# Performance work log

Hardware: AMD Instinct MI355X
Metric: run time of the kernel (lower is better)

The kernel has to match this reference:

```python
import jax, jax.numpy as jnp
import numpy as np

HEADS = 24
HEAD_DIM = 96
SPARSE_N = 4
ROPE_FREQ = 10000.0


def _rope_axis(x, pos, scale):
    # x: (s, b, h, D) with D even; pos: (s,) integer positions along one axis
    D = x.shape[-1]
    inv_freq = 1.0 / (ROPE_FREQ ** (jnp.arange(0, D, 2, dtype=jnp.float32) / D))
    t = pos.astype(jnp.float32) / scale
    freqs = t[:, None] * inv_freq[None, :]            # (s, D/2)
    emb = jnp.concatenate([freqs, freqs], axis=-1)    # (s, D)
    cos = jnp.cos(emb)[:, None, None, :]              # broadcast over (b, h)
    sin = jnp.sin(emb)[:, None, None, :]
    x1, x2 = jnp.split(x, 2, axis=-1)
    rot = jnp.concatenate([-x2, x1], axis=-1)         # rotate_half
    return x * cos + rot * sin


def _rope3d(x, frame, height, width, scales=(1.0, 1.0, 1.0)):
    # x: (s, b, h, d); head dim is split into 3 equal chunks for t/h/w axes
    s, b, h, d = x.shape
    D = d // 3
    tt, hh, ww = jnp.meshgrid(jnp.arange(frame), jnp.arange(height), jnp.arange(width), indexing='ij')
    pos_t, pos_h, pos_w = tt.reshape(-1), hh.reshape(-1), ww.reshape(-1)
    return jnp.concatenate([
        _rope_axis(x[..., :D], pos_t, scales[0]),
        _rope_axis(x[..., D:2 * D], pos_h, scales[1]),
        _rope_axis(x[..., 2 * D:], pos_w, scales[2]),
    ], axis=-1)


def setup_inputs() -> dict:
    key = jax.random.key(0)
    ks = jax.random.split(key, 9)
    frame, height, width, b = 8, 16, 16, 4
    s = frame * height * width          # 2048
    dim = HEADS * HEAD_DIM              # 2304
    w_scale = 0.02
    return {
        'hidden_states': jax.random.normal(ks[0], (s, b, dim), jnp.float32),
        'wq': jax.random.normal(ks[1], (dim, dim), jnp.float32) * w_scale,
        'bq': jnp.zeros((dim,), jnp.float32),
        'wk': jax.random.normal(ks[2], (dim, dim), jnp.float32) * w_scale,
        'bk': jnp.zeros((dim,), jnp.float32),
        'wv': jax.random.normal(ks[3], (dim, dim), jnp.float32) * w_scale,
        'bv': jnp.zeros((dim,), jnp.float32),
        'wo': jax.random.normal(ks[4], (dim, dim), jnp.float32) * w_scale,
        'bo': jnp.zeros((dim,), jnp.float32),
        'frame': frame,
        'height': height,
        'width': width,
    }


def reference(hidden_states, wq, bq, wk, bk, wv, bv, wo, bo, frame, height, width):
    # hidden_states: (s, b, dim) in SBH layout, self-attention path (no seq-parallel)
    s, b, dim = hidden_states.shape
    n = SPARSE_N

    q = hidden_states @ wq + bq
    k = hidden_states @ wk + bk
    v = hidden_states @ wv + bv

    # 3D RoPE on q/k, per-head
    q = _rope3d(q.reshape(s, b, HEADS, HEAD_DIM), frame, height, width).reshape(s, b, dim)
    k = _rope3d(k.reshape(s, b, HEADS, HEAD_DIM), frame, height, width).reshape(s, b, dim)

    # _sparse_1d (sparse_group=False): pad s to multiple of n*n, then
    # '(g k) b d -> g (k b) d' == contiguous reshape
    pad_len = (-s) % (n * n)
    sp_s = (s + pad_len) // n
    sp_b = n * b

    def sparse(x):
        if pad_len:
            x = jnp.pad(x, ((0, pad_len), (0, 0), (0, 0)))
        return x.reshape(sp_s, sp_b, dim)

    q, k, v = sparse(q), sparse(k), sparse(v)

    # 's b (h d) -> b h s d'
    def to_bhsd(x):
        return x.reshape(sp_s, sp_b, HEADS, HEAD_DIM).transpose(1, 2, 0, 3)

    qh, kh, vh = to_bhsd(q), to_bhsd(k), to_bhsd(v)

    # scaled dot-product attention (no mask, no dropout, non-causal)
    scale = HEAD_DIM ** -0.5
    scores = jnp.einsum('bhqd,bhkd->bhqk', qh, kh) * scale
    attn = jax.nn.softmax(scores, axis=-1)
    out = jnp.einsum('bhqk,bhkd->bhqd', attn, vh)

    # 'b h s d -> s b (h d)', reverse sparse rearrange, drop padding
    out = out.transpose(2, 0, 1, 3).reshape(sp_s, sp_b, dim)
    out = out.reshape(sp_s * n, b, dim)[:s]

    # to_out[0] linear, to_out[1] dropout (identity in eval), rescale_output_factor=1
    return out @ wo + bo
```

## Files before the change

### kernel.cpp

```cpp
#include <hip/hip_runtime.h>
#include <hip/hip_bf16.h>

typedef __attribute__((ext_vector_type(8))) __bf16 bf16x8;
typedef __attribute__((ext_vector_type(4))) __bf16 bf16x4;
typedef __attribute__((ext_vector_type(4))) float  f32x4;

#define DIM   2304
#define NH    24
#define HD    96
#define SPS   512

__device__ __forceinline__ void gload16(const void* gp, void* lp) {
  __builtin_amdgcn_global_load_lds(
      (__attribute__((address_space(1))) void*)(unsigned long long)gp,
      (__attribute__((address_space(3))) void*)lp, 16, 0, 0);
}

__global__ __launch_bounds__(256) void pack_w_kernel(
    const float* __restrict__ wq, const float* __restrict__ wk,
    const float* __restrict__ wv, const float* __restrict__ wo,
    __bf16* __restrict__ dqkv, __bf16* __restrict__ dwo)
{
  __shared__ float t[64][65];
  const int z = blockIdx.z;
  const float* src = (z == 0) ? wq : (z == 1) ? wk : (z == 2) ? wv : wo;
  __bf16* dst = (z < 3) ? (dqkv + (size_t)z * DIM * DIM) : dwo;
  const int n0 = blockIdx.x * 64, k0 = blockIdx.y * 64;
  const int tx = threadIdx.x & 63, ty = threadIdx.x >> 6;
#pragma unroll
  for (int j = 0; j < 64; j += 4)
    t[ty + j][tx] = src[(size_t)(k0 + ty + j) * DIM + n0 + tx];
  __syncthreads();
#pragma unroll
  for (int j = 0; j < 64; j += 4)
    dst[(size_t)(n0 + ty + j) * DIM + k0 + tx] = (__bf16)t[tx][ty + j];
}

__global__ __launch_bounds__(256) void pack_hs_kernel(
    const float4* __restrict__ src, bf16x4* __restrict__ dst)
{
  const int i = blockIdx.x * 256 + threadIdx.x;
  const float4 f = src[i];
  bf16x4 o = { (__bf16)f.x, (__bf16)f.y, (__bf16)f.z, (__bf16)f.w };
  dst[i] = o;
}


template<int NJ>
__device__ __forceinline__ void stage_half(
    const __bf16* __restrict__ X, __bf16* lX, int r0, int k0,
    int srow, int schunk, int dslot)
{
#pragma unroll
  for (int j = 0; j < NJ; ++j)
    gload16(X + (size_t)(r0 + j * 64 + srow) * DIM + k0 + schunk,
            lX + (j * 64 + srow) * 64 + dslot);
}

template<int MF, int H, int Q, bool LA, bool LB>
__device__ __forceinline__ void phase8(
    const char* ab, const char* bb, int wm, int wn, int laneA0, int laneA1,
    bf16x8 (&a)[MF][2], bf16x8 (&bq)[2][2][2], f32x4 (&acc)[2 * MF][4])
{
  if (LA) {
#pragma unroll
    for (int fm = 0; fm < MF; ++fm) {
      a[fm][0] = *(const bf16x8*)(ab + (wm * (MF * 32) + H * (MF * 16) + fm * 16) * 128 + laneA0);
      a[fm][1] = *(const bf16x8*)(ab + (wm * (MF * 32) + H * (MF * 16) + fm * 16) * 128 + laneA1);
    }
  }
  if (LB) {
#pragma unroll
    for (int fn = 0; fn < 2; ++fn) {
      bq[Q][fn][0] = *(const bf16x8*)(bb + (wn * 64 + Q * 32 + fn * 16) * 128 + laneA0);
      bq[Q][fn][1] = *(const bf16x8*)(bb + (wn * 64 + Q * 32 + fn * 16) * 128 + laneA1);
    }
  }
  __builtin_amdgcn_s_barrier();
  asm volatile("s_waitcnt lgkmcnt(0)" ::: "memory");
  __builtin_amdgcn_s_setprio(1);
#pragma unroll
  for (int fm = 0; fm < MF; ++fm)
#pragma unroll
    for (int fn = 0; fn < 2; ++fn)
#pragma unroll
      for (int kk = 0; kk < 2; ++kk)
        acc[H * MF + fm][Q * 2 + fn] = __builtin_amdgcn_mfma_f32_16x16x32_bf16(
            a[fm][kk], bq[Q][fn][kk], acc[H * MF + fm][Q * 2 + fn], 0, 0, 0);
  __builtin_amdgcn_s_setprio(0);
  __builtin_amdgcn_s_barrier();
}

template<int EPI>
__global__ __launch_bounds__(512, 2) void gemm8p_kernel(
    const __bf16* __restrict__ A, const __bf16* __restrict__ B,
    const float* __restrict__ b0, const float* __restrict__ b1, const float* __restrict__ b2,
    __bf16* __restrict__ o0, __bf16* __restrict__ o1, __bf16* __restrict__ o2,
    float* __restrict__ fout)
{
  constexpr int MF = (EPI == 0) ? 4 : 2;
  constexpr int MROWS = MF * 64;
  __shared__ __align__(16) __bf16 As[2][MROWS * 64];
  __shared__ __align__(16) __bf16 Bs[2][256 * 64];
  __shared__ float tcos[640], tsin[640];
  const int tid = threadIdx.x;
  if (EPI == 0) {
    for (int i = tid; i < 640; i += 512) {
      int pos, jj = i & 15;
      if (i < 128)      pos = i >> 4;
      else if (i < 384) pos = (i - 128) >> 4;
      else              pos = (i - 384) >> 4;
      const float invf = exp2f(-(float)jj * 0.83048202372184059f);
      float s, c;
      sincosf((float)pos * invf, &s, &c);
      tcos[i] = c; tsin[i] = s;
    }
  }
  const int wid = tid >> 6, l = tid & 63;
  const int lq = l & 15, lg = l >> 4;
  const int wm = wid >> 2, wn = wid & 3;
  const int bid = blockIdx.x;
  const int xcd = bid & 7, local = bid >> 3;
  int m0, n0;
  if (EPI == 0) {
    m0 = (xcd * 4 + (local & 3)) * 256;
    n0 = (local >> 2) * 256;
  } else {
    m0 = (xcd * 8 + (local & 7)) * 128;
    n0 = (local >> 3) * 256;
  }
  const int srow = tid >> 3;
  const int schunk = ((tid & 7) ^ (srow & 7)) * 8;
  const int dslot = (tid & 7) * 8;
  const int laneA0 = lq * 128 + ((lg * 16) ^ ((lq & 7) << 4));
  const int laneA1 = lq * 128 + ((64 + lg * 16) ^ ((lq & 7) << 4));

  f32x4 acc[2 * MF][4] = {};
  bf16x8 a[MF][2], bq[2][2][2];

  stage_half<MF>(A, As[0], m0, 0, srow, schunk, dslot);
  stage_half<4>(B, Bs[0], n0, 0, srow, schunk, dslot);
  stage_half<MF>(A, As[1], m0, 64, srow, schunk, dslot);
  stage_half<4>(B, Bs[1], n0, 64, srow, schunk, dslot);
  if (EPI == 0) asm volatile("s_waitcnt vmcnt(8)" ::: "memory");
  else          asm volatile("s_waitcnt vmcnt(6)" ::: "memory");
  __builtin_amdgcn_s_barrier();

  const char* a0p = (const char*)&As[0][0];
  const char* b0p = (const char*)&Bs[0][0];
  const char* a1p = (const char*)&As[1][0];
  const char* b1p = (const char*)&Bs[1][0];

#define TILE_STAGED(AP, BP, SA, SB, KN)                                          \
  phase8<MF, 0, 0, true,  true >(AP, BP, wm, wn, laneA0, laneA1, a, bq, acc);    \
  phase8<MF, 0, 1, false, true >(AP, BP, wm, wn, laneA0, laneA1, a, bq, acc);    \
  stage_half<4>(B, SB, n0, KN, srow, schunk, dslot);                             \
  phase8<MF, 1, 1, true,  false>(AP, BP, wm, wn, laneA0, laneA1, a, bq, acc);    \
  stage_half<MF>(A, SA, m0, KN, srow, schunk, dslot);                            \
  phase8<MF, 1, 0, false, false>(AP, BP, wm, wn, laneA0, laneA1, a, bq, acc);    \
  if (EPI == 0) asm volatile("s_waitcnt vmcnt(8)" ::: "memory");                 \
  else          asm volatile("s_waitcnt vmcnt(6)" ::: "memory");                 \
  __builtin_amdgcn_s_barrier();

#define TILE_PLAIN(AP, BP)                                                       \
  phase8<MF, 0, 0, true,  true >(AP, BP, wm, wn, laneA0, laneA1, a, bq, acc);    \
  phase8<MF, 0, 1, false, true >(AP, BP, wm, wn, laneA0, laneA1, a, bq, acc);    \
  phase8<MF, 1, 1, true,  false>(AP, BP, wm, wn, laneA0, laneA1, a, bq, acc);    \
  phase8<MF, 1, 0, false, false>(AP, BP, wm, wn, laneA0, laneA1, a, bq, acc);

  for (int tt = 0; tt < 34; tt += 2) {
    TILE_STAGED(a0p, b0p, As[0], Bs[0], (tt + 2) * 64)
    TILE_STAGED(a1p, b1p, As[1], Bs[1], (tt + 3) * 64)
  }
  TILE_PLAIN(a0p, b0p)
  asm volatile("s_waitcnt vmcnt(0)" ::: "memory");
  __builtin_amdgcn_s_barrier();
  TILE_PLAIN(a1p, b1p)
#undef TILE_STAGED
#undef TILE_PLAIN

  if (EPI == 0) {
    const int mat = n0 / DIM;
    const int nb = n0 - mat * DIM;
    const float* bias = (mat == 0) ? b0 : (mat == 1) ? b1 : b2;
    __bf16* outp = (mat == 0) ? o0 : (mat == 1) ? o1 : o2;
#pragma unroll
    for (int mr = 0; mr < 8; ++mr) {
      const int gq = (m0 + wm * 128 + mr * 16) >> 4;
      const int si = gq * 4 + lg;
      const int pos3[3] = { si >> 8, (si >> 4) & 15, si & 15 };
#pragma unroll
      for (int p = 0; p < 2; ++p) {
        const int nlo = nb + wn * 64 + (2 * p) * 16 + lq;
        const int nhi = nlo + 16;
        const int hlo = nlo / HD, dlo = nlo - hlo * HD;
        const int hhi = nhi / HD, dhi = nhi - hhi * HD;
        const float blo = bias[nlo], bhi = bias[nhi];
        float c = 1.f, s = 0.f;
        if (mat < 2) {
          const int cix = dlo >> 5;
          const int toff = ((cix == 0) ? 0 : (cix == 1) ? 128 : 384) + pos3[cix] * 16 + lq;
          c = tcos[toff]; s = tsin[toff];
        }
#pragma unroll
        for (int r = 0; r < 4; ++r) {
          const int bp = lg * 4 + r;
          const float x1 = acc[mr][2 * p][r] + blo;
          const float x2 = acc[mr][2 * p + 1][r] + bhi;
          float y1 = x1, y2 = x2;
          if (mat < 2) { y1 = x1 * c - x2 * s; y2 = x2 * c + x1 * s; }
          outp[((size_t)(bp * NH + hlo) * SPS + gq) * HD + dlo] = (__bf16)y1;
          outp[((size_t)(bp * NH + hhi) * SPS + gq) * HD + dhi] = (__bf16)y2;
        }
      }
    }
  } else {
#pragma unroll
    for (int mr = 0; mr < 4; ++mr) {
      const int rbase = m0 + wm * 64 + mr * 16;
#pragma unroll
      for (int nr = 0; nr < 4; ++nr) {
        const int n = n0 + wn * 64 + nr * 16 + lq;
        const float bia = b0[n];
#pragma unroll
        for (int r = 0; r < 4; ++r)
          fout[(size_t)(rbase + lg * 4 + r) * DIM + n] = acc[mr][nr][r] + bia;
      }
    }
  }
}

__global__ __launch_bounds__(256) void attn_kernel(
    const __bf16* __restrict__ q, const __bf16* __restrict__ k,
    const __bf16* __restrict__ v, __bf16* __restrict__ ao)
{
  __shared__ __bf16 Vt[96 * 72];
  __shared__ __bf16 Pl[4][16 * 72];
  const int tid = threadIdx.x;
  const int w = tid >> 6, l = tid & 63;
  const int lq = l & 15, lg = l >> 4;
  const int bid = blockIdx.x;
  const int swz = (bid & 7) * 384 + (bid >> 3);
  const int qt = swz & 7;
  const int h  = (swz >> 3) % NH;
  const int bp = swz / (NH * 8);
  const size_t bh = ((size_t)bp * NH + h) * SPS;
  const __bf16* qb = q + bh * HD;
  const __bf16* kb = k + bh * HD;
  const __bf16* vb = v + bh * HD;
  bf16x8 qf[3];
  {
    const __bf16* qr = qb + (size_t)(qt * 64 + w * 16 + lq) * HD + lg * 8;
    qf[0] = *(const bf16x8*)(qr);
    qf[1] = *(const bf16x8*)(qr + 32);
    qf[2] = *(const bf16x8*)(qr + 64);
  }
  const float sc = 0.10206207261596575f * 1.4426950408889634f;
  float m_run = -1e30f, l_run = 0.f;
  f32x4 o[6] = {};
  for (int kb0 = 0; kb0 < SPS; kb0 += 64) {
    __syncthreads();
#pragma unroll
    for (int p = 0; p < 3; ++p) {
      const int lin = p * 256 + tid;
      const int row = lin / 12, c8 = (lin % 12) * 8;
      bf16x8 vv = *(const bf16x8*)(vb + (size_t)(kb0 + row) * HD + c8);
#pragma unroll
      for (int j = 0; j < 8; ++j) Vt[(c8 + j) * 72 + row] = vv[j];
    }
    __syncthreads();
    f32x4 st[4];
#pragma unroll
    for (int t2 = 0; t2 < 4; ++t2) {
      const __bf16* kr = kb + (size_t)(kb0 + t2 * 16 + lq) * HD + lg * 8;
      bf16x8 k0f = *(const bf16x8*)(kr);
      bf16x8 k1f = *(const bf16x8*)(kr + 32);
      bf16x8 k2f = *(const bf16x8*)(kr + 64);
      f32x4 s = {};
      s = __builtin_amdgcn_mfma_f32_16x16x32_bf16(k0f, qf[0], s, 0, 0, 0);
      s = __builtin_amdgcn_mfma_f32_16x16x32_bf16(k1f, qf[1], s, 0, 0, 0);
      s = __builtin_amdgcn_mfma_f32_16x16x32_bf16(k2f, qf[2], s, 0, 0, 0);
      st[t2] = s;
    }
    float tmax = -1e30f;
#pragma unroll
    for (int t2 = 0; t2 < 4; ++t2)
#pragma unroll
      for (int r = 0; r < 4; ++r) tmax = fmaxf(tmax, st[t2][r]);
    tmax = fmaxf(tmax, __shfl_xor(tmax, 16));
    tmax = fmaxf(tmax, __shfl_xor(tmax, 32));
    tmax *= sc;
    const float m_new = fmaxf(m_run, tmax);
    const float alpha = exp2f(m_run - m_new);
    float tsum = 0.f;
#pragma unroll
    for (int t2 = 0; t2 < 4; ++t2) {
      bf16x4 pb;
#pragma unroll
      for (int r = 0; r < 4; ++r) {
        const float p = exp2f(st[t2][r] * sc - m_new);
        tsum += p;
        pb[r] = (__bf16)p;
      }
      *(bf16x4*)&Pl[w][lq * 72 + t2 * 16 + lg * 4] = pb;
    }
    tsum += __shfl_xor(tsum, 16);
    tsum += __shfl_xor(tsum, 32);
    l_run = l_run * alpha + tsum;
    m_run = m_new;
    float al[4];
#pragma unroll
    for (int r = 0; r < 4; ++r) al[r] = __shfl(alpha, lg * 4 + r);
#pragma unroll
    for (int ni = 0; ni < 6; ++ni)
#pragma unroll
      for (int r = 0; r < 4; ++r) o[ni][r] *= al[r];
#pragma unroll
    for (int ks = 0; ks < 2; ++ks) {
      bf16x8 pa = *(const bf16x8*)&Pl[w][lq * 72 + ks * 32 + lg * 8];
#pragma unroll
      for (int ni = 0; ni < 6; ++ni) {
        bf16x8 vf = *(const bf16x8*)&Vt[(ni * 16 + lq) * 72 + ks * 32 + lg * 8];
        o[ni] = __builtin_amdgcn_mfma_f32_16x16x32_bf16(pa, vf, o[ni], 0, 0, 0);
      }
    }
  }
  float linv[4];
#pragma unroll
  for (int r = 0; r < 4; ++r) linv[r] = 1.f / __shfl(l_run, lg * 4 + r);
#pragma unroll
  for (int ni = 0; ni < 6; ++ni)
#pragma unroll
    for (int r = 0; r < 4; ++r) {
      const int gq = qt * 64 + w * 16 + lg * 4 + r;
      const int d = ni * 16 + lq;
      ao[(size_t)(gq * 16 + bp) * DIM + h * HD + d] = (__bf16)(o[ni][r] * linv[r]);
    }
}

extern "C" void kernel_launch(void* const* d_in, const int* in_sizes, int n_in,
                              void* d_out, int out_size, void* d_ws, size_t ws_size,
                              hipStream_t stream) {
  const float* hs = (const float*)d_in[0];
  const float* wq = (const float*)d_in[1];
  const float* bq = (const float*)d_in[2];
  const float* wk = (const float*)d_in[3];
  const float* bk = (const float*)d_in[4];
  const float* wv = (const float*)d_in[5];
  const float* bv = (const float*)d_in[6];
  const float* wo = (const float*)d_in[7];
  const float* bo = (const float*)d_in[8];
  float* out = (float*)d_out;

  char* ws = (char*)d_ws;
  __bf16* wqkvT = (__bf16*)(ws);
  __bf16* woT   = (__bf16*)(ws + 31850496);
  __bf16* hsb   = (__bf16*)(ws + 42467328);
  __bf16* qb    = (__bf16*)(ws + 80216064);
  __bf16* kbuf  = (__bf16*)(ws + 117964800);
  __bf16* vbuf  = (__bf16*)(ws + 155713536);
  __bf16* ao    = hsb;

  pack_w_kernel<<<dim3(36, 36, 4), 256, 0, stream>>>(wq, wk, wv, wo, wqkvT, woT);
  pack_hs_kernel<<<18432, 256, 0, stream>>>((const float4*)hs, (bf16x4*)hsb);
  gemm8p_kernel<0><<<864, 512, 0, stream>>>(hsb, wqkvT, bq, bk, bv, qb, kbuf, vbuf, nullptr);
  attn_kernel<<<3072, 256, 0, stream>>>(qb, kbuf, vbuf, ao);
  gemm8p_kernel<1><<<576, 512, 0, stream>>>(ao, woT, bo, nullptr, nullptr, nullptr, nullptr, nullptr, out);
}
```

Before: 570.6 us.

## Software-pipeline LDS fragment loads across MFMA phases in GEMM main loop

The per-phase load→barrier→wait-all→MFMA structure is replaced by a software-pipelined schedule. The next A/B fragments are read from LDS while the current MFMAs run, using double-buffered register sets, partial lgkmcnt waits and sched_barrier fences to pin the instruction order. Launch bounds drop from 2 to 1 block per CU so the extra live fragment registers fit. This aims to hide LDS latency behind matrix math, at the cost of lower occupancy and a more fragile hand-counted wait schedule.

```diff
diff --git a/kernel.cpp b/kernel.cpp
--- a/kernel.cpp
+++ b/kernel.cpp
@@ -9,6 +9,11 @@
 #define NH    24
 #define HD    96
 #define SPS   512
+
+#define SBAR() __builtin_amdgcn_sched_barrier(0)
+#define BARR() __builtin_amdgcn_s_barrier()
+#define LGKM(n) asm volatile("s_waitcnt lgkmcnt(%0)" :: "n"(n) : "memory")
+#define VMC(n)  asm volatile("s_waitcnt vmcnt(%0)"  :: "n"(n) : "memory")
 
 __device__ __forceinline__ void gload16(const void* gp, void* lp) {
   __builtin_amdgcn_global_load_lds(
@@ -57,49 +62,21 @@
             lX + (j * 64 + srow) * 64 + dslot);
 }
 
-template<int MF, int H, int Q, bool LA, bool LB>
-__device__ __forceinline__ void phase8(
-    const char* ab, const char* bb, int wm, int wn, int laneA0, int laneA1,
-    bf16x8 (&a)[MF][2], bf16x8 (&bq)[2][2][2], f32x4 (&acc)[2 * MF][4])
-{
-  if (LA) {
-#pragma unroll
-    for (int fm = 0; fm < MF; ++fm) {
-      a[fm][0] = *(const bf16x8*)(ab + (wm * (MF * 32) + H * (MF * 16) + fm * 16) * 128 + laneA0);
-      a[fm][1] = *(const bf16x8*)(ab + (wm * (MF * 32) + H * (MF * 16) + fm * 16) * 128 + laneA1);
-    }
-  }
-  if (LB) {
-#pragma unroll
-    for (int fn = 0; fn < 2; ++fn) {
-      bq[Q][fn][0] = *(const bf16x8*)(bb + (wn * 64 + Q * 32 + fn * 16) * 128 + laneA0);
-      bq[Q][fn][1] = *(const bf16x8*)(bb + (wn * 64 + Q * 32 + fn * 16) * 128 + laneA1);
-    }
-  }
-  __builtin_amdgcn_s_barrier();
-  asm volatile("s_waitcnt lgkmcnt(0)" ::: "memory");
-  __builtin_amdgcn_s_setprio(1);
-#pragma unroll
-  for (int fm = 0; fm < MF; ++fm)
-#pragma unroll
-    for (int fn = 0; fn < 2; ++fn)
-#pragma unroll
-      for (int kk = 0; kk < 2; ++kk)
-        acc[H * MF + fm][Q * 2 + fn] = __builtin_amdgcn_mfma_f32_16x16x32_bf16(
-            a[fm][kk], bq[Q][fn][kk], acc[H * MF + fm][Q * 2 + fn], 0, 0, 0);
-  __builtin_amdgcn_s_setprio(0);
-  __builtin_amdgcn_s_barrier();
-}
-
 template<int EPI>
-__global__ __launch_bounds__(512, 2) void gemm8p_kernel(
+__global__ __launch_bounds__(512, 1) void gemm8p_kernel(
     const __bf16* __restrict__ A, const __bf16* __restrict__ B,
-    const float* __restrict__ b0, const float* __restrict__ b1, const float* __restrict__ b2,
+    const float* __restrict__ b0, const float* __restrict__ b1v, const float* __restrict__ b2,
     __bf16* __restrict__ o0, __bf16* __restrict__ o1, __bf16* __restrict__ o2,
     float* __restrict__ fout)
 {
   constexpr int MF = (EPI == 0) ? 4 : 2;
   constexpr int MROWS = MF * 64;
+  constexpr int AL = 2 * MF;
+  constexpr int L_P0 = AL + 4;
+  constexpr int L_P1 = AL;
+  constexpr int L_P2 = AL + 4;
+  constexpr int V_PRO = MF + 4;
+
   __shared__ __align__(16) __bf16 As[2][MROWS * 64];
   __shared__ __align__(16) __bf16 Bs[2][256 * 64];
   __shared__ float tcos[640], tsin[640];
@@ -115,6 +92,7 @@
       sincosf((float)pos * invf, &s, &c);
       tcos[i] = c; tsin[i] = s;
     }
+    LGKM(0);
   }
   const int wid = tid >> 6, l = tid & 63;
   const int lq = l & 15, lg = l >> 4;
@@ -136,56 +114,80 @@
   const int laneA1 = lq * 128 + ((64 + lg * 16) ^ ((lq & 7) << 4));
 
   f32x4 acc[2 * MF][4] = {};
-  bf16x8 a[MF][2], bq[2][2][2];
+  bf16x8 aX[MF][2], aY[MF][2], b0A[2][2], b0B[2][2], b1[2][2];
+
+#define LOAD_A(dst, bufp, Hh) do { _Pragma("unroll")                            \
+  for (int fm = 0; fm < MF; ++fm) {                                             \
+    dst[fm][0] = *(const bf16x8*)((bufp) + (wm * (MF * 32) + (Hh) * (MF * 16) + fm * 16) * 128 + laneA0); \
+    dst[fm][1] = *(const bf16x8*)((bufp) + (wm * (MF * 32) + (Hh) * (MF * 16) + fm * 16) * 128 + laneA1); } } while (0)
+
+#define LOAD_B(dst, bufp, Qq) do { _Pragma("unroll")                            \
+  for (int fn = 0; fn < 2; ++fn) {                                              \
+    dst[fn][0] = *(const bf16x8*)((bufp) + (wn * 64 + (Qq) * 32 + fn * 16) * 128 + laneA0); \
+    dst[fn][1] = *(const bf16x8*)((bufp) + (wn * 64 + (Qq) * 32 + fn * 16) * 128 + laneA1); } } while (0)
+
+#define MFMA8(aset, bset, Hh, Qq) do {                                          \
+  __builtin_amdgcn_s_setprio(1); _Pragma("unroll")                              \
+  for (int fm = 0; fm < MF; ++fm) _Pragma("unroll")                             \
+    for (int fn = 0; fn < 2; ++fn) _Pragma("unroll")                            \
+      for (int kk = 0; kk < 2; ++kk)                                            \
+        acc[(Hh) * MF + fm][(Qq) * 2 + fn] = __builtin_amdgcn_mfma_f32_16x16x32_bf16( \
+            aset[fm][kk], bset[fn][kk], acc[(Hh) * MF + fm][(Qq) * 2 + fn], 0, 0, 0); \
+  __builtin_amdgcn_s_setprio(0); } while (0)
 
   stage_half<MF>(A, As[0], m0, 0, srow, schunk, dslot);
   stage_half<4>(B, Bs[0], n0, 0, srow, schunk, dslot);
   stage_half<MF>(A, As[1], m0, 64, srow, schunk, dslot);
   stage_half<4>(B, Bs[1], n0, 64, srow, schunk, dslot);
-  if (EPI == 0) asm volatile("s_waitcnt vmcnt(8)" ::: "memory");
-  else          asm volatile("s_waitcnt vmcnt(6)" ::: "memory");
-  __builtin_amdgcn_s_barrier();
-
+  VMC(V_PRO);
+  BARR();
   const char* a0p = (const char*)&As[0][0];
   const char* b0p = (const char*)&Bs[0][0];
   const char* a1p = (const char*)&As[1][0];
   const char* b1p = (const char*)&Bs[1][0];
-
-#define TILE_STAGED(AP, BP, SA, SB, KN)                                          \
-  phase8<MF, 0, 0, true,  true >(AP, BP, wm, wn, laneA0, laneA1, a, bq, acc);    \
-  phase8<MF, 0, 1, false, true >(AP, BP, wm, wn, laneA0, laneA1, a, bq, acc);    \
-  stage_half<4>(B, SB, n0, KN, srow, schunk, dslot);                             \
-  phase8<MF, 1, 1, true,  false>(AP, BP, wm, wn, laneA0, laneA1, a, bq, acc);    \
-  stage_half<MF>(A, SA, m0, KN, srow, schunk, dslot);                            \
-  phase8<MF, 1, 0, false, false>(AP, BP, wm, wn, laneA0, laneA1, a, bq, acc);    \
-  if (EPI == 0) asm volatile("s_waitcnt vmcnt(8)" ::: "memory");                 \
-  else          asm volatile("s_waitcnt vmcnt(6)" ::: "memory");                 \
-  __builtin_amdgcn_s_barrier();
-
-#define TILE_PLAIN(AP, BP)                                                       \
-  phase8<MF, 0, 0, true,  true >(AP, BP, wm, wn, laneA0, laneA1, a, bq, acc);    \
-  phase8<MF, 0, 1, false, true >(AP, BP, wm, wn, laneA0, laneA1, a, bq, acc);    \
-  phase8<MF, 1, 1, true,  false>(AP, BP, wm, wn, laneA0, laneA1, a, bq, acc);    \
-  phase8<MF, 1, 0, false, false>(AP, BP, wm, wn, laneA0, laneA1, a, bq, acc);
+  LOAD_A(aX, a0p, 0);
+  LOAD_B(b0A, b0p, 0);
+  LOAD_B(b1, b0p, 1);
+  SBAR();
+
+#define STEADY_TILE(ACURP, BCURP, ANXTP, BNXTP, SADST, SBDST, B0CUR, B0NXT, KNOFF, DOSTG, GATEN) \
+  BARR(); LOAD_A(aY, ACURP, 1); SBAR(); LGKM(L_P0); SBAR(); MFMA8(aX, B0CUR, 0, 0);  \
+  BARR(); SBAR(); LGKM(L_P1); SBAR(); MFMA8(aX, b1, 0, 1);                            \
+  BARR();                                                                              \
+  if (DOSTG) stage_half<4>(B, SBDST, n0, KNOFF, srow, schunk, dslot);                  \
+  VMC(GATEN); BARR();                                                                  \
+  LOAD_A(aX, ANXTP, 0); LOAD_B(B0NXT, BNXTP, 0); SBAR(); LGKM(L_P2); SBAR();           \
+  MFMA8(aY, b1, 1, 1);                                                                 \
+  BARR();                                                                              \
+  if (DOSTG) stage_half<MF>(A, SADST, m0, KNOFF, srow, schunk, dslot);                 \
+  LOAD_B(b1, BNXTP, 1); SBAR(); MFMA8(aY, B0CUR, 1, 0);
+
+#define FINAL_TILE(ACURP, B0CUR)                                                      \
+  BARR(); LOAD_A(aY, ACURP, 1); SBAR(); LGKM(L_P0); SBAR(); MFMA8(aX, B0CUR, 0, 0);  \
+  BARR(); SBAR(); LGKM(L_P1); SBAR(); MFMA8(aX, b1, 0, 1);                            \
+  BARR(); SBAR(); LGKM(0); SBAR(); MFMA8(aY, b1, 1, 1);                               \
+  BARR(); SBAR(); MFMA8(aY, B0CUR, 1, 0);
 
   for (int tt = 0; tt < 34; tt += 2) {
-    TILE_STAGED(a0p, b0p, As[0], Bs[0], (tt + 2) * 64)
-    TILE_STAGED(a1p, b1p, As[1], Bs[1], (tt + 3) * 64)
-  }
-  TILE_PLAIN(a0p, b0p)
-  asm volatile("s_waitcnt vmcnt(0)" ::: "memory");
-  __builtin_amdgcn_s_barrier();
-  TILE_PLAIN(a1p, b1p)
-#undef TILE_STAGED
-#undef TILE_PLAIN
+    STEADY_TILE(a0p, b0p, a1p, b1p, As[0], Bs[0], b0A, b0B, (tt + 2) * 64, 1, 4)
+    STEADY_TILE(a1p, b1p, a0p, b0p, As[1], Bs[1], b0B, b0A, (tt + 3) * 64, 1, 4)
+  }
+  STEADY_TILE(a0p, b0p, a1p, b1p, As[0], Bs[0], b0A, b0B, 0, 0, 0)
+  FINAL_TILE(a1p, b0B)
+
+#undef STEADY_TILE
+#undef FINAL_TILE
+#undef LOAD_A
+#undef LOAD_B
+#undef MFMA8
 
   if (EPI == 0) {
     const int mat = n0 / DIM;
     const int nb = n0 - mat * DIM;
-    const float* bias = (mat == 0) ? b0 : (mat == 1) ? b1 : b2;
+    const float* bias = (mat == 0) ? b0 : (mat == 1) ? b1v : b2;
     __bf16* outp = (mat == 0) ? o0 : (mat == 1) ? o1 : o2;
 #pragma unroll
-    for (int mr = 0; mr < 8; ++mr) {
+    for (int mr = 0; mr < 2 * MF; ++mr) {
       const int gq = (m0 + wm * 128 + mr * 16) >> 4;
       const int si = gq * 4 + lg;
       const int pos3[3] = { si >> 8, (si >> 4) & 15, si & 15 };
@@ -216,7 +218,7 @@
     }
   } else {
 #pragma unroll
-    for (int mr = 0; mr < 4; ++mr) {
+    for (int mr = 0; mr < 2 * MF; ++mr) {
       const int rbase = m0 + wm * 64 + mr * 16;
 #pragma unroll
       for (int nr = 0; nr < 4; ++nr) {
```

Result: slower. 1.558 ms (+173.0%).

## Store V transposed from QKV GEMM and read it directly in attention

Applied to the files above, without the earlier changes.

The QKV projection epilogue now writes V in a head-dim-major (transposed) layout, so the attention kernel can load V fragments straight from global memory instead of staging and transposing them through shared memory. This removes the per-tile V transpose and its two block barriers. MFMA sections are also wrapped in s_setprio to favour matrix issue. The costs are strided 2-byte scattered stores in the GEMM epilogue for V, and repeated global (L2) reads of V by every wave without LDS reuse.

```diff
diff --git a/kernel.cpp b/kernel.cpp
--- a/kernel.cpp
+++ b/kernel.cpp
@@ -209,8 +209,13 @@
           const float x2 = acc[mr][2 * p + 1][r] + bhi;
           float y1 = x1, y2 = x2;
           if (mat < 2) { y1 = x1 * c - x2 * s; y2 = x2 * c + x1 * s; }
-          outp[((size_t)(bp * NH + hlo) * SPS + gq) * HD + dlo] = (__bf16)y1;
-          outp[((size_t)(bp * NH + hhi) * SPS + gq) * HD + dhi] = (__bf16)y2;
+          if (mat == 2) {
+            outp[((size_t)(bp * NH + hlo) * HD + dlo) * SPS + gq] = (__bf16)y1;
+            outp[((size_t)(bp * NH + hhi) * HD + dhi) * SPS + gq] = (__bf16)y2;
+          } else {
+            outp[((size_t)(bp * NH + hlo) * SPS + gq) * HD + dlo] = (__bf16)y1;
+            outp[((size_t)(bp * NH + hhi) * SPS + gq) * HD + dhi] = (__bf16)y2;
+          }
         }
       }
     }
@@ -232,9 +237,8 @@
 
 __global__ __launch_bounds__(256) void attn_kernel(
     const __bf16* __restrict__ q, const __bf16* __restrict__ k,
-    const __bf16* __restrict__ v, __bf16* __restrict__ ao)
-{
-  __shared__ __bf16 Vt[96 * 72];
+    const __bf16* __restrict__ vT, __bf16* __restrict__ ao)
+{
   __shared__ __bf16 Pl[4][16 * 72];
   const int tid = threadIdx.x;
   const int w = tid >> 6, l = tid & 63;
@@ -244,10 +248,10 @@
   const int qt = swz & 7;
   const int h  = (swz >> 3) % NH;
   const int bp = swz / (NH * 8);
-  const size_t bh = ((size_t)bp * NH + h) * SPS;
-  const __bf16* qb = q + bh * HD;
-  const __bf16* kb = k + bh * HD;
-  const __bf16* vb = v + bh * HD;
+  const size_t bh = (size_t)bp * NH + h;
+  const __bf16* qb = q + bh * SPS * HD;
+  const __bf16* kb = k + bh * SPS * HD;
+  const __bf16* vb = vT + bh * HD * SPS;
   bf16x8 qf[3];
   {
     const __bf16* qr = qb + (size_t)(qt * 64 + w * 16 + lq) * HD + lg * 8;
@@ -259,17 +263,8 @@
   float m_run = -1e30f, l_run = 0.f;
   f32x4 o[6] = {};
   for (int kb0 = 0; kb0 < SPS; kb0 += 64) {
-    __syncthreads();
-#pragma unroll
-    for (int p = 0; p < 3; ++p) {
-      const int lin = p * 256 + tid;
-      const int row = lin / 12, c8 = (lin % 12) * 8;
-      bf16x8 vv = *(const bf16x8*)(vb + (size_t)(kb0 + row) * HD + c8);
-#pragma unroll
-      for (int j = 0; j < 8; ++j) Vt[(c8 + j) * 72 + row] = vv[j];
-    }
-    __syncthreads();
     f32x4 st[4];
+    __builtin_amdgcn_s_setprio(1);
 #pragma unroll
     for (int t2 = 0; t2 < 4; ++t2) {
       const __bf16* kr = kb + (size_t)(kb0 + t2 * 16 + lq) * HD + lg * 8;
@@ -282,6 +277,7 @@
       s = __builtin_amdgcn_mfma_f32_16x16x32_bf16(k2f, qf[2], s, 0, 0, 0);
       st[t2] = s;
     }
+    __builtin_amdgcn_s_setprio(0);
     float tmax = -1e30f;
 #pragma unroll
     for (int t2 = 0; t2 < 4; ++t2)
@@ -318,11 +314,13 @@
 #pragma unroll
     for (int ks = 0; ks < 2; ++ks) {
       bf16x8 pa = *(const bf16x8*)&Pl[w][lq * 72 + ks * 32 + lg * 8];
+      __builtin_amdgcn_s_setprio(1);
 #pragma unroll
       for (int ni = 0; ni < 6; ++ni) {
-        bf16x8 vf = *(const bf16x8*)&Vt[(ni * 16 + lq) * 72 + ks * 32 + lg * 8];
+        bf16x8 vf = *(const bf16x8*)(vb + (size_t)(ni * 16 + lq) * SPS + kb0 + ks * 32 + lg * 8);
         o[ni] = __builtin_amdgcn_mfma_f32_16x16x32_bf16(pa, vf, o[ni], 0, 0, 0);
       }
+      __builtin_amdgcn_s_setprio(0);
     }
   }
   float linv[4];
@@ -358,12 +356,12 @@
   __bf16* hsb   = (__bf16*)(ws + 42467328);
   __bf16* qb    = (__bf16*)(ws + 80216064);
   __bf16* kbuf  = (__bf16*)(ws + 117964800);
-  __bf16* vbuf  = (__bf16*)(ws + 155713536);
+  __bf16* vbufT = (__bf16*)(ws + 155713536);
   __bf16* ao    = hsb;
 
   pack_w_kernel<<<dim3(36, 36, 4), 256, 0, stream>>>(wq, wk, wv, wo, wqkvT, woT);
   pack_hs_kernel<<<18432, 256, 0, stream>>>((const float4*)hs, (bf16x4*)hsb);
-  gemm8p_kernel<0><<<864, 512, 0, stream>>>(hsb, wqkvT, bq, bk, bv, qb, kbuf, vbuf, nullptr);
-  attn_kernel<<<3072, 256, 0, stream>>>(qb, kbuf, vbuf, ao);
+  gemm8p_kernel<0><<<864, 512, 0, stream>>>(hsb, wqkvT, bq, bk, bv, qb, kbuf, vbufT, nullptr);
+  attn_kernel<<<3072, 256, 0, stream>>>(qb, kbuf, vbufT, ao);
   gemm8p_kernel<1><<<576, 512, 0, stream>>>(ao, woT, bo, nullptr, nullptr, nullptr, nullptr, nullptr, out);
 }
```

Result: slower. 767.7 us (+34.5%).
